# Kernel optimization log

Measured on AMD Instinct MI355X. Metric: run time of the kernel, lower is better.

## Reference

```python
import jax, jax.numpy as jnp
import numpy as np

B, T, HID = 1, 256, 2048
H, D = 16, 128
KD = H * D
CONV = 4
MAX_CG = 30
LAMB_LB = 0.25
NORM_EPS = 1e-5


def setup_inputs() -> dict:
    key = jax.random.key(0)
    ks = jax.random.split(key, 10)
    s = 0.02
    init_lamb = float(np.log(np.exp(1.0 - LAMB_LB) - 1.0))  # softplus^-1(1 - lower_bound)
    return {
        "hidden_states": jax.random.normal(ks[0], (B, T, HID), jnp.float32),
        "Wq": jax.random.normal(ks[1], (HID, KD), jnp.float32) * s,
        "Wk": jax.random.normal(ks[2], (HID, KD), jnp.float32) * s,
        "Wv": jax.random.normal(ks[3], (HID, KD), jnp.float32) * s,
        "Wa": jax.random.normal(ks[4], (HID, H), jnp.float32) * s,
        "ba": jnp.full((H,), 2.0, jnp.float32),
        "Wb": jax.random.normal(ks[5], (HID, H), jnp.float32) * s,
        "bb": jnp.zeros((H,), jnp.float32),
        "conv_wq": jax.random.normal(ks[6], (KD, CONV), jnp.float32) * s,
        "conv_wk": jax.random.normal(ks[7], (KD, CONV), jnp.float32) * s,
        "lambda_params": jnp.full((KD,), init_lamb, jnp.float32),
        "o_norm_w": jnp.ones((D,), jnp.float32),
        "Wo": jax.random.normal(ks[8], (KD, HID), jnp.float32) * s,
    }


def short_conv_silu(x, w):
    # depthwise causal conv over time; x [b,t,c], w [c,k]
    k = w.shape[1]
    xp = jnp.pad(x, ((0, 0), (k - 1, 0), (0, 0)))
    t = x.shape[1]
    y = xp[:, 0:t, :] * w[:, 0]
    for i in range(1, k):
        y = y + xp[:, i:i + t, :] * w[:, i]
    return jax.nn.silu(y)


def l2norm(x):
    return x * jax.lax.rsqrt(jnp.sum(x * x, -1, keepdims=True) + 1e-6)


def rmsnorm(x, w):
    return x * jax.lax.rsqrt(jnp.mean(x * x, -1, keepdims=True) + NORM_EPS) * w


def cg_solve(A, b):
    # solve A x = b per (batch, head) with fixed CG iterations, x0 = 0
    matvec = lambda p: jnp.einsum('bhij,bhj->bhi', A, p)
    x0 = jnp.zeros_like(b)
    rs0 = jnp.sum(b * b, -1)

    def body(i, st):
        xc, r, p, rs = st
        Ap = matvec(p)
        alpha = rs / (jnp.sum(p * Ap, -1) + 1e-12)
        xc = xc + alpha[..., None] * p
        r = r - alpha[..., None] * Ap
        rs_n = jnp.sum(r * r, -1)
        p = r + (rs_n / (rs + 1e-12))[..., None] * p
        return xc, r, p, rs_n

    xf, _, _, _ = jax.lax.fori_loop(0, MAX_CG, body, (x0, b, b, rs0))
    return xf


def mesa_recurrence(q, k, v, g, beta, lamb_diag):
    # q,k,v [b,t,h,d]; g,beta [b,t,h]; lamb_diag [h,d,d]
    def step(carry, inp):
        h_kk, h_kv = carry
        qt, kt, vt, gt, bt = inp
        decay = jnp.exp(gt)[..., None, None]
        b_ = bt[..., None, None]
        h_kk = h_kk * decay + b_ * (kt[..., :, None] * kt[..., None, :])
        h_kv = h_kv * decay + b_ * (kt[..., :, None] * vt[..., None, :])
        A = h_kk + lamb_diag[None]
        q_star = cg_solve(A, qt)
        ot = jnp.einsum('bhk,bhkv->bhv', q_star, h_kv)
        return (h_kk, h_kv), ot

    init = (jnp.zeros((B, H, D, D), q.dtype), jnp.zeros((B, H, D, D), q.dtype))
    xs = (q.transpose(1, 0, 2, 3), k.transpose(1, 0, 2, 3), v.transpose(1, 0, 2, 3),
          g.transpose(1, 0, 2), beta.transpose(1, 0, 2))
    _, o = jax.lax.scan(step, init, xs)
    return o.transpose(1, 0, 2, 3)  # [b,t,h,d]


def reference(hidden_states, Wq, Wk, Wv, Wa, ba, Wb, bb, conv_wq, conv_wk,
              lambda_params, o_norm_w, Wo):
    x = hidden_states
    q = short_conv_silu(x @ Wq, conv_wq)
    k = short_conv_silu(x @ Wk, conv_wk)
    v = x @ Wv
    q = l2norm(q.reshape(B, T, H, D))
    k = l2norm(k.reshape(B, T, H, D))
    v = v.reshape(B, T, H, D)
    beta = jax.nn.sigmoid(x @ Wb + bb)          # [b,t,h]
    g = jax.nn.log_sigmoid(x @ Wa + ba)          # [b,t,h]
    lamb = (jax.nn.softplus(lambda_params) + LAMB_LB).reshape(H, D)
    lamb_diag = lamb[:, :, None] * jnp.eye(D, dtype=lamb.dtype)  # [h,d,d]
    o = mesa_recurrence(q, k, v, g, beta, lamb_diag)
    o = rmsnorm(o, o_norm_w)
    o = o.reshape(B, T, KD) @ Wo
    return o
```

## Files before the change

### kernel.cpp

```cpp
#include <hip/hip_runtime.h>
#include <math.h>

#define TT 256
#define HIDDEN 2048
#define NH 16
#define HD 128
#define KDIM 2048
#define NCG 30

typedef _Float16 h4 __attribute__((ext_vector_type(4)));
typedef _Float16 half8 __attribute__((ext_vector_type(8)));
typedef float floatx4 __attribute__((ext_vector_type(4)));

__device__ __forceinline__ half8 cvt8(const float4 x, const float4 y) {
    half8 f;
    f[0] = (_Float16)x.x; f[1] = (_Float16)x.y; f[2] = (_Float16)x.z; f[3] = (_Float16)x.w;
    f[4] = (_Float16)y.x; f[5] = (_Float16)y.y; f[6] = (_Float16)y.z; f[7] = (_Float16)y.w;
    return f;
}

__device__ __forceinline__ void glds16(const void* g, void* l) {
    __builtin_amdgcn_global_load_lds(
        (const __attribute__((address_space(1))) void*)g,
        (__attribute__((address_space(3))) void*)l, 16, 0, 0);
}

#define SBAR() __builtin_amdgcn_sched_barrier(0)

#define ASTR 72
#define GEMM_LDS (3 * 64 * 128 * 4 + 2 * 64 * ASTR * 2)

__global__ __launch_bounds__(256) void gemm_kernel(
    const float* __restrict__ A,
    const float* __restrict__ Wq, const float* __restrict__ Wk,
    const float* __restrict__ Wv,
    const float* __restrict__ Wa, const float* __restrict__ Wb,
    float* __restrict__ C0, float* __restrict__ C1, float* __restrict__ C2,
    const float* __restrict__ ba, const float* __restrict__ bb,
    float* __restrict__ g, float* __restrict__ beta)
{
    extern __shared__ char smem[];
    float* Bf = (float*)smem;
    _Float16* Ash = (_Float16*)(smem + 3 * 64 * 128 * 4);

    const int tid = threadIdx.x, lane = tid & 63, w = tid >> 6;
    const int q = lane >> 4, l16 = lane & 15;

    const int b = blockIdx.x;
    const int xcd = b & 7, gslot = b >> 3;
    int nt, mt;
    if (gslot < 24) { nt = xcd * 6 + (gslot >> 2); mt = gslot & 3; }
    else           { nt = 48;                      mt = xcd; }
    const int mat = nt >> 4;
    const int ntile = nt & 15;
    const int n0 = ntile * 128;
    const float* __restrict__ W = (mat == 0) ? Wq : (mat == 1) ? Wk : (mat == 2) ? Wv : Wa;
    float* __restrict__ C = (mat == 0) ? C0 : (mat == 1) ? C1 : C2;
    const int m0 = mt * 64;

    const int ar = tid >> 2, ac = (tid & 3) * 16;
    const float* __restrict__ Ap = &A[(size_t)(m0 + ar) * KDIM + ac];

    floatx4 acc[4][2] = {};
    float4 a0, a1, a2, a3;
    float bab[16];

    auto stageB = [&](int s, int buf) {
#pragma unroll
        for (int i = 0; i < 8; i++) {
            const int r0 = w * 16 + i * 2;
            const int row = r0 + (lane >> 5);
            const int qr = (r0 >> 3) & 3;
            const int c = (((lane & 31) * 4) + 128 - 8 * qr) & 127;
            glds16(&W[(size_t)(s * 64 + row) * KDIM + n0 + c],
                   &Bf[(buf * 64 + r0) * 128]);
        }
    };
    auto loadA = [&](int s) {
        a0 = *(const float4*)&Ap[s * 64];      a1 = *(const float4*)&Ap[s * 64 + 4];
        a2 = *(const float4*)&Ap[s * 64 + 8];  a3 = *(const float4*)&Ap[s * 64 + 12];
    };
    auto writeA = [&](int buf) {
        *(half8*)&Ash[buf * 64 * ASTR + ar * ASTR + ac] = cvt8(a0, a1);
        *(half8*)&Ash[buf * 64 * ASTR + ar * ASTR + ac + 8] = cvt8(a2, a3);
    };
    auto loadBab = [&](int s) {
        if (w >= 2) return;
        const float* __restrict__ Wsrc = (w == 0) ? Wa : Wb;
        const int hh = lane & 15, ko = lane >> 4;
#pragma unroll
        for (int hf = 0; hf < 2; hf++)
#pragma unroll
            for (int j = 0; j < 8; j++)
                bab[hf * 8 + j] = Wsrc[(size_t)(s * 64 + hf * 32 + ko * 8 + j) * NH + hh];
    };
    auto writeBab = [&](int buf) {
        if (w >= 2) return;
        const int hh = lane & 15, ko = lane >> 4;
        const int col = w * 16 + hh;
        const int cp = (col + 8 * ko) & 127;
#pragma unroll
        for (int hf = 0; hf < 2; hf++)
#pragma unroll
            for (int j = 0; j < 8; j++)
                Bf[(buf * 64 + hf * 32 + ko * 8 + j) * 128 + cp] = bab[hf * 8 + j];
    };

    const int NSTEP = KDIM / 64;

#define GEMM_COMPUTE(BBASE, ABASE)                                                          \
    {                                                                                       \
    const int c0s = (w * 32 + l16 + 8 * q) & 127;                                           \
    const int c1s = (w * 32 + 16 + l16 + 8 * q) & 127;                                      \
    _Pragma("unroll")                                                                       \
    for (int kk = 0; kk < 2; kk++) {                                                        \
        float f0[8], f1[8];                                                                 \
        _Pragma("unroll")                                                                   \
        for (int j = 0; j < 8; j++) {                                                       \
            const int rowb = ((BBASE) + kk * 32 + q * 8 + j) * 128;                         \
            f0[j] = Bf[rowb + c0s];                                                         \
            f1[j] = Bf[rowb + c1s];                                                         \
        }                                                                                   \
        const half8 bf0 = cvt8(*(const float4*)&f0[0], *(const float4*)&f0[4]);             \
        const half8 bf1 = cvt8(*(const float4*)&f1[0], *(const float4*)&f1[4]);             \
        _Pragma("unroll")                                                                   \
        for (int rr = 0; rr < 4; rr++) {                                                    \
            const half8 af = *(const half8*)&Ash[(ABASE) + (rr * 16 + l16) * ASTR + kk * 32 + q * 8]; \
            acc[rr][0] = __builtin_amdgcn_mfma_f32_16x16x32_f16(af, bf0, acc[rr][0], 0, 0, 0); \
            acc[rr][1] = __builtin_amdgcn_mfma_f32_16x16x32_f16(af, bf1, acc[rr][1], 0, 0, 0); \
        }                                                                                   \
    }                                                                                       \
    }

    if (mat == 3) {
        for (int i = tid; i < 2 * 64 * 96; i += 256) {
            const int buf = i / 6144;
            const int rest = i - buf * 6144;
            const int row = rest / 96, c = 32 + (rest - row * 96);
            const int cp = (c + 8 * ((row >> 3) & 3)) & 127;
            Bf[(buf * 64 + row) * 128 + cp] = 0.f;
        }
        loadBab(0); writeBab(0); loadBab(1);
        loadA(0); writeA(0); loadA(1);
        __syncthreads();
        for (int s = 0; s < NSTEP; s++) {
            const int cur = s & 1;
            GEMM_COMPUTE(cur * 64, cur * 64 * ASTR);
            if (s + 1 < NSTEP) {
                writeBab(cur ^ 1);
                if (s + 2 < NSTEP) loadBab(s + 2);
                writeA(cur ^ 1);
                if (s + 2 < NSTEP) loadA(s + 2);
            }
            __syncthreads();
        }
        if (w == 0) {
            const float bav = ba[l16], bbv = bb[l16];
#pragma unroll
            for (int rr = 0; rr < 4; rr++)
#pragma unroll
                for (int r = 0; r < 4; r++) {
                    const int tr = m0 + rr * 16 + q * 4 + r;
                    float z0 = acc[rr][0][r] + bav;
                    g[tr * NH + l16] = fminf(z0, 0.f) - log1pf(__expf(-fabsf(z0)));
                    float z1 = acc[rr][1][r] + bbv;
                    beta[tr * NH + l16] = 1.f / (1.f + __expf(-z1));
                }
        }
        return;
    }

    stageB(0, 0);
    SBAR();
    loadA(0); writeA(0);
    SBAR();
    loadA(1);
    SBAR();
    stageB(1, 1);
    SBAR();

    for (int s = 0; s < NSTEP; s++) {
        if (s < NSTEP - 1) { asm volatile("s_waitcnt vmcnt(12) lgkmcnt(0)" ::: "memory"); }
        else               { asm volatile("s_waitcnt vmcnt(0) lgkmcnt(0)" ::: "memory"); }
        SBAR();
        __builtin_amdgcn_s_barrier();
        SBAR();
        if (s + 1 < NSTEP) writeA((s + 1) & 1);
        SBAR();
        if (s + 2 < NSTEP) loadA(s + 2);
        SBAR();
        if (s + 2 < NSTEP) stageB(s + 2, (s + 2) % 3);
        GEMM_COMPUTE((s % 3) * 64, (s & 1) * 64 * ASTR);
    }

#pragma unroll
    for (int rr = 0; rr < 4; rr++)
#pragma unroll
        for (int r = 0; r < 4; r++) {
            const int row = m0 + rr * 16 + q * 4 + r;
            C[(size_t)row * KDIM + n0 + w * 32 + l16] = acc[rr][0][r];
            C[(size_t)row * KDIM + n0 + w * 32 + 16 + l16] = acc[rr][1][r];
        }
#undef GEMM_COMPUTE
}

__global__ __launch_bounds__(256) void gemm64_kernel(
    const float* __restrict__ A, const float* __restrict__ Wo,
    float* __restrict__ C)
{
    __shared__ __align__(16) float Bf[3][64][64];
    __shared__ __align__(16) _Float16 Ash[2][32 * ASTR];

    const int tid = threadIdx.x, lane = tid & 63, w = tid >> 6;
    const int q = lane >> 4, l16 = lane & 15;
    const int b = blockIdx.x;
    const int xcd = b & 7, gslot = b >> 3;
    const int nt = xcd * 4 + (gslot >> 3), mt = gslot & 7;
    const int n0 = nt * 64, m0 = mt * 32;

    const int ar = tid >> 3, ac = (tid & 7) * 8;
    const float* __restrict__ Ap = &A[(size_t)(m0 + ar) * KDIM + ac];

    floatx4 acc0 = {}, acc1 = {};
    float4 ax, ay;

    auto stageB = [&](int s, int buf) {
#pragma unroll
        for (int i = 0; i < 4; i++) {
            const int r0 = w * 16 + i * 4;
            const int row = r0 + (lane >> 4);
            const int qr = (r0 >> 3) & 3;
            const int c = (((lane & 15) * 4) + 64 - 8 * qr) & 63;
            glds16(&Wo[(size_t)(s * 64 + row) * KDIM + n0 + c],
                   &Bf[buf][r0][0]);
        }
    };
    auto loadA = [&](int s) {
        ax = *(const float4*)&Ap[s * 64];
        ay = *(const float4*)&Ap[s * 64 + 4];
    };
    auto writeA = [&](int buf) {
        *(half8*)&Ash[buf][ar * ASTR + ac] = cvt8(ax, ay);
    };

    stageB(0, 0);
    SBAR();
    loadA(0); writeA(0);
    SBAR();
    loadA(1);
    SBAR();
    stageB(1, 1);
    SBAR();

    const int NSTEP = KDIM / 64;
    for (int s = 0; s < NSTEP; s++) {
        if (s < NSTEP - 1) { asm volatile("s_waitcnt vmcnt(6) lgkmcnt(0)" ::: "memory"); }
        else               { asm volatile("s_waitcnt vmcnt(0) lgkmcnt(0)" ::: "memory"); }
        SBAR();
        __builtin_amdgcn_s_barrier();
        SBAR();
        if (s + 1 < NSTEP) writeA((s + 1) & 1);
        SBAR();
        if (s + 2 < NSTEP) loadA(s + 2);
        SBAR();
        if (s + 2 < NSTEP) stageB(s + 2, (s + 2) % 3);
        const int bb = s % 3, ab = s & 1;
        const int c0s = (w * 16 + l16 + 8 * q) & 63;
#pragma unroll
        for (int kk = 0; kk < 2; kk++) {
            float f[8];
#pragma unroll
            for (int j = 0; j < 8; j++)
                f[j] = Bf[bb][kk * 32 + q * 8 + j][c0s];
            const half8 bf  = cvt8(*(const float4*)&f[0], *(const float4*)&f[4]);
            const half8 af0 = *(const half8*)&Ash[ab][l16 * ASTR + kk * 32 + q * 8];
            const half8 af1 = *(const half8*)&Ash[ab][(16 + l16) * ASTR + kk * 32 + q * 8];
            acc0 = __builtin_amdgcn_mfma_f32_16x16x32_f16(af0, bf, acc0, 0, 0, 0);
            acc1 = __builtin_amdgcn_mfma_f32_16x16x32_f16(af1, bf, acc1, 0, 0, 0);
        }
    }

#pragma unroll
    for (int r = 0; r < 4; r++) {
        C[(size_t)(m0 + q * 4 + r) * KDIM + n0 + w * 16 + l16] = acc0[r];
        C[(size_t)(m0 + 16 + q * 4 + r) * KDIM + n0 + w * 16 + l16] = acc1[r];
    }
}

__global__ __launch_bounds__(256) void conv_silu_l2_kernel(
    const float* __restrict__ q_pre, const float* __restrict__ k_pre,
    const float* __restrict__ cwq, const float* __restrict__ cwk,
    float* __restrict__ qn, float* __restrict__ kn)
{
    const int t = blockIdx.x, h = blockIdx.y;
    const int which = threadIdx.x >> 7, d = threadIdx.x & 127;
    const int w = threadIdx.x >> 6;
    const int c = h * HD + d;
    const float* pre = which ? k_pre : q_pre;
    const float* cw  = which ? cwk : cwq;
    float y = 0.f;
#pragma unroll
    for (int i = 0; i < 4; i++) {
        const int ts = t - 3 + i;
        if (ts >= 0) y = fmaf(pre[ts * KDIM + c], cw[c * 4 + i], y);
    }
    const float s = y / (1.f + __expf(-y));
    float v = s * s;
#pragma unroll
    for (int off = 32; off > 0; off >>= 1) v += __shfl_down(v, off, 64);
    __shared__ float red[4];
    if ((threadIdx.x & 63) == 0) red[w] = v;
    __syncthreads();
    const float sum = red[which * 2] + red[which * 2 + 1];
    float* dst = which ? kn : qn;
    dst[t * KDIM + c] = s * rsqrtf(sum + 1e-6f);
}

#define PSTR 136
#define YSTR 264

template<int SMAX>
__device__ __forceinline__ void mesa_cg(
    const float* __restrict__ qn, const float* __restrict__ kn, const float* __restrict__ vv,
    const float* __restrict__ g, const float* __restrict__ bet, const float* __restrict__ lp,
    const float* __restrict__ onw, float* __restrict__ out,
    int h, int t0, _Float16* Psh, _Float16* Ysh, float* red,
    float* Gsh, float* bets)
{
    constexpr int NSUB1 = SMAX / 64;
    constexpr int NK2   = SMAX / 32;

    const int tid = threadIdx.x, lane = tid & 63, w = tid >> 6;
    const int quad = lane >> 4, l16 = lane & 15;
    const int tmy = t0 + l16;
    const int dbase = w * 32;

    {
        float sc = g[tid * NH + h];
#pragma unroll
        for (int off = 1; off < 64; off <<= 1) {
            const float o = __shfl_up(sc, off, 64);
            if (lane >= off) sc += o;
        }
        if (lane == 63) red[w] = sc;
        bets[tid] = bet[tid * NH + h];
        __syncthreads();
        float woff = 0.f;
        for (int u = 0; u < w; u++) woff += red[u];
        Gsh[tid] = sc + woff;
        __syncthreads();
    }

    half8 K1[NSUB1][4];
#pragma unroll
    for (int ii = 0; ii < NSUB1; ii++) {
        const int srow = 16 * (w + 4 * ii) + l16;
        const float* kp = &kn[(srow * NH + h) * HD];
#pragma unroll
        for (int kk = 0; kk < 4; kk++) {
            const float4 a = *(const float4*)&kp[kk * 32 + quad * 8];
            const float4 b = *(const float4*)&kp[kk * 32 + quad * 8 + 4];
            K1[ii][kk] = cvt8(a, b);
        }
    }

    half8 KtF[2][NK2];
#pragma unroll
    for (int ss = 0; ss < 2; ss++) {
        const int d = dbase + ss * 16 + l16;
#pragma unroll
        for (int kk = 0; kk < NK2; kk++) {
#pragma unroll
            for (int j = 0; j < 8; j++) {
                const int s = kk * 32 + quad * 8 + j;
                KtF[ss][kk][j] = (_Float16)kn[(s * NH + h) * HD + d];
            }
        }
    }

    half8 Vf[NK2][2];
#pragma unroll
    for (int kk = 0; kk < NK2; kk++) {
#pragma unroll
        for (int ss = 0; ss < 2; ss++) {
            const int dv = dbase + ss * 16 + l16;
#pragma unroll
            for (int j = 0; j < 8; j++) {
                const int s = kk * 32 + quad * 8 + j;
                Vf[kk][ss][j] = (_Float16)vv[(s * NH + h) * HD + dv];
            }
        }
    }

    const float Gt = Gsh[tmy];
    float Wm[NSUB1][4];
#pragma unroll
    for (int ii = 0; ii < NSUB1; ii++)
#pragma unroll
        for (int r = 0; r < 4; r++) {
            const int s = 16 * (w + 4 * ii) + quad * 4 + r;
            Wm[ii][r] = (s <= tmy) ? bets[s] * __expf(Gt - Gsh[s]) : 0.f;
        }
    float lam[8], xv[8], rv[8], pv[8];
#pragma unroll
    for (int ss = 0; ss < 2; ss++)
#pragma unroll
        for (int r = 0; r < 4; r++) {
            const int e = ss * 4 + r;
            const int d = dbase + ss * 16 + quad * 4 + r;
            const float lx = lp[h * HD + d];
            lam[e] = fmaxf(lx, 0.f) + log1pf(__expf(-fabsf(lx))) + 0.25f;
            const float b = qn[(tmy * NH + h) * HD + d];
            xv[e] = 0.f; rv[e] = b; pv[e] = b;
        }
    float rs = 0.f;
#pragma unroll
    for (int e = 0; e < 8; e++) rs += rv[e] * rv[e];
    rs += __shfl_xor(rs, 16, 64); rs += __shfl_xor(rs, 32, 64);

    auto writeP = [&](const float* src) {
#pragma unroll
        for (int ss = 0; ss < 2; ss++) {
            h4 ph;
            ph.x = (_Float16)src[ss * 4 + 0]; ph.y = (_Float16)src[ss * 4 + 1];
            ph.z = (_Float16)src[ss * 4 + 2]; ph.w = (_Float16)src[ss * 4 + 3];
            *(h4*)&Psh[l16 * PSTR + dbase + ss * 16 + quad * 4] = ph;
        }
    };
    writeP(pv);

    for (int it = 0; it <= NCG; it++) {
        __syncthreads();
        floatx4 acc1a[NSUB1] = {}, acc1b[NSUB1] = {};
#pragma unroll
        for (int kk = 0; kk < 2; kk++) {
            const half8 bfa = *(const half8*)&Psh[l16 * PSTR + kk * 32 + quad * 8];
            const half8 bfb = *(const half8*)&Psh[l16 * PSTR + (kk + 2) * 32 + quad * 8];
#pragma unroll
            for (int ii = 0; ii < NSUB1; ii++) {
                acc1a[ii] = __builtin_amdgcn_mfma_f32_16x16x32_f16(K1[ii][kk], bfa, acc1a[ii], 0, 0, 0);
                acc1b[ii] = __builtin_amdgcn_mfma_f32_16x16x32_f16(K1[ii][kk + 2], bfb, acc1b[ii], 0, 0, 0);
            }
        }
#pragma unroll
        for (int ii = 0; ii < NSUB1; ii++) {
            h4 yh;
            yh.x = (_Float16)(Wm[ii][0] * (acc1a[ii][0] + acc1b[ii][0]));
            yh.y = (_Float16)(Wm[ii][1] * (acc1a[ii][1] + acc1b[ii][1]));
            yh.z = (_Float16)(Wm[ii][2] * (acc1a[ii][2] + acc1b[ii][2]));
            yh.w = (_Float16)(Wm[ii][3] * (acc1a[ii][3] + acc1b[ii][3]));
            *(h4*)&Ysh[l16 * YSTR + 16 * (w + 4 * ii) + quad * 4] = yh;
        }
        __syncthreads();
        if (it == NCG) break;

        floatx4 acc2a[2] = {}, acc2b[2] = {};
#pragma unroll
        for (int kk = 0; kk < NK2; kk += 2) {
            const half8 bf0 = *(const half8*)&Ysh[l16 * YSTR + kk * 32 + quad * 8];
            const half8 bf1 = *(const half8*)&Ysh[l16 * YSTR + (kk + 1) * 32 + quad * 8];
#pragma unroll
            for (int ss = 0; ss < 2; ss++) {
                acc2a[ss] = __builtin_amdgcn_mfma_f32_16x16x32_f16(KtF[ss][kk], bf0, acc2a[ss], 0, 0, 0);
                acc2b[ss] = __builtin_amdgcn_mfma_f32_16x16x32_f16(KtF[ss][kk + 1], bf1, acc2b[ss], 0, 0, 0);
            }
        }
        float Ap[8], pAp = 0.f;
#pragma unroll
        for (int ss = 0; ss < 2; ss++)
#pragma unroll
            for (int r = 0; r < 4; r++) {
                const int e = ss * 4 + r;
                Ap[e] = (acc2a[ss][r] + acc2b[ss][r]) + lam[e] * pv[e];
                pAp = fmaf(pv[e], Ap[e], pAp);
            }
        pAp += __shfl_xor(pAp, 16, 64); pAp += __shfl_xor(pAp, 32, 64);
        const float alpha = rs / (pAp + 1e-12f);
        float rsn = 0.f;
#pragma unroll
        for (int e = 0; e < 8; e++) {
            xv[e] = fmaf(alpha, pv[e], xv[e]);
            rv[e] = fmaf(-alpha, Ap[e], rv[e]);
            rsn = fmaf(rv[e], rv[e], rsn);
        }
        rsn += __shfl_xor(rsn, 16, 64); rsn += __shfl_xor(rsn, 32, 64);
        const float bcg = rsn / (rs + 1e-12f);
#pragma unroll
        for (int e = 0; e < 8; e++) pv[e] = fmaf(bcg, pv[e], rv[e]);
        rs = rsn;
        writeP(it == NCG - 1 ? xv : pv);
    }

    floatx4 accOa[2] = {}, accOb[2] = {};
#pragma unroll
    for (int kk = 0; kk < NK2; kk += 2) {
        const half8 af0 = *(const half8*)&Ysh[l16 * YSTR + kk * 32 + quad * 8];
        const half8 af1 = *(const half8*)&Ysh[l16 * YSTR + (kk + 1) * 32 + quad * 8];
#pragma unroll
        for (int ss = 0; ss < 2; ss++) {
            accOa[ss] = __builtin_amdgcn_mfma_f32_16x16x32_f16(af0, Vf[kk][ss], accOa[ss], 0, 0, 0);
            accOb[ss] = __builtin_amdgcn_mfma_f32_16x16x32_f16(af1, Vf[kk + 1][ss], accOb[ss], 0, 0, 0);
        }
    }
    float accO[2][4];
#pragma unroll
    for (int ss = 0; ss < 2; ss++)
#pragma unroll
        for (int r = 0; r < 4; r++) accO[ss][r] = accOa[ss][r] + accOb[ss][r];

    float part[4];
#pragma unroll
    for (int r = 0; r < 4; r++) {
        part[r] = accO[0][r] * accO[0][r] + accO[1][r] * accO[1][r];
#pragma unroll
        for (int off = 1; off < 16; off <<= 1) part[r] += __shfl_xor(part[r], off, 64);
    }
    if (l16 == 0) {
#pragma unroll
        for (int r = 0; r < 4; r++) red[w * 16 + quad * 4 + r] = part[r];
    }
    __syncthreads();
    const float w0 = onw[dbase + l16], w1 = onw[dbase + 16 + l16];
#pragma unroll
    for (int r = 0; r < 4; r++) {
        const int qr = quad * 4 + r;
        const float sumd = red[qr] + red[16 + qr] + red[32 + qr] + red[48 + qr];
        const float sc = rsqrtf(sumd * (1.f / HD) + 1e-5f);
        const int trow = ((t0 + qr) * NH + h) * HD;
        out[trow + dbase + l16] = accO[0][r] * sc * w0;
        out[trow + dbase + 16 + l16] = accO[1][r] * sc * w1;
    }
}

__global__ __launch_bounds__(256, 1) void mesa_kernel(
    const float* __restrict__ qn, const float* __restrict__ kn, const float* __restrict__ vv,
    const float* __restrict__ g, const float* __restrict__ bet, const float* __restrict__ lp,
    const float* __restrict__ onw, float* __restrict__ out)
{
    __shared__ __align__(16) _Float16 Psh[16 * PSTR];
    __shared__ __align__(16) _Float16 Ysh[16 * YSTR];
    __shared__ float red[64];
    __shared__ float Gsh[256];
    __shared__ float bets[256];
    const int h = blockIdx.x, jb = blockIdx.y, t0 = jb * 16;
    switch (jb >> 2) {
        case 0:  mesa_cg<64> (qn, kn, vv, g, bet, lp, onw, out, h, t0, Psh, Ysh, red, Gsh, bets); break;
        case 1:  mesa_cg<128>(qn, kn, vv, g, bet, lp, onw, out, h, t0, Psh, Ysh, red, Gsh, bets); break;
        case 2:  mesa_cg<192>(qn, kn, vv, g, bet, lp, onw, out, h, t0, Psh, Ysh, red, Gsh, bets); break;
        default: mesa_cg<256>(qn, kn, vv, g, bet, lp, onw, out, h, t0, Psh, Ysh, red, Gsh, bets); break;
    }
}

extern "C" void kernel_launch(void* const* d_in, const int* in_sizes, int n_in,
                              void* d_out, int out_size, void* d_ws, size_t ws_size,
                              hipStream_t stream)
{
    (void)in_sizes; (void)n_in; (void)out_size; (void)ws_size;
    const float* x   = (const float*)d_in[0];
    const float* Wq  = (const float*)d_in[1];
    const float* Wk  = (const float*)d_in[2];
    const float* Wv  = (const float*)d_in[3];
    const float* Wa  = (const float*)d_in[4];
    const float* ba  = (const float*)d_in[5];
    const float* Wb  = (const float*)d_in[6];
    const float* bb  = (const float*)d_in[7];
    const float* cwq = (const float*)d_in[8];
    const float* cwk = (const float*)d_in[9];
    const float* lp  = (const float*)d_in[10];
    const float* onw = (const float*)d_in[11];
    const float* Wo  = (const float*)d_in[12];

    char* wsb = (char*)d_ws;
    float* q_pre = (float*)wsb;
    float* k_pre = q_pre + 524288;
    float* v     = k_pre + 524288;
    float* qn    = v + 524288;
    float* kn    = qn + 524288;
    float* g     = kn + 524288;
    float* beta  = g + 4096;
    float* onorm = q_pre;
    float* outp  = (float*)d_out;

    (void)hipFuncSetAttribute((const void*)gemm_kernel,
                              hipFuncAttributeMaxDynamicSharedMemorySize, GEMM_LDS);
    gemm_kernel<<<dim3(196), 256, GEMM_LDS, stream>>>(x, Wq, Wk, Wv, Wa, Wb,
                                                      q_pre, k_pre, v, ba, bb, g, beta);
    conv_silu_l2_kernel<<<dim3(TT, NH), 256, 0, stream>>>(q_pre, k_pre, cwq, cwk, qn, kn);

    mesa_kernel<<<dim3(NH, 16), 256, 0, stream>>>(qn, kn, v, g, beta, lp, onw, onorm);

    gemm64_kernel<<<dim3(256), 256, 0, stream>>>(onorm, Wo, outp);
}
```

Measured before the change: 228.7 us.

## Fuse causal conv, SiLU and L2 norm into the mesa CG kernel

Removes the separate conv_silu_l2 kernel and recomputes the short convolution, SiLU and L2 normalisation of k (for rows up to SMAX) and q (for the block's 16 rows) inside each mesa block. The normalised k is staged as fp16 in dynamic LDS and q as fp32 in LDS, so the normalised tensors are never written to or read back from global memory and one launch disappears. In exchange every block redundantly recomputes k's convolution with a serial two-pass loop per row, which adds latency at the start of each block, and LDS use grows considerably.

After: 267.5 us. 1.17x slower.

```diff
diff --git a/kernel.cpp b/kernel.cpp
--- a/kernel.cpp
+++ b/kernel.cpp
@@ -287,45 +287,24 @@
     }
 }
 
-__global__ __launch_bounds__(256) void conv_silu_l2_kernel(
-    const float* __restrict__ q_pre, const float* __restrict__ k_pre,
-    const float* __restrict__ cwq, const float* __restrict__ cwk,
-    float* __restrict__ qn, float* __restrict__ kn)
-{
-    const int t = blockIdx.x, h = blockIdx.y;
-    const int which = threadIdx.x >> 7, d = threadIdx.x & 127;
-    const int w = threadIdx.x >> 6;
-    const int c = h * HD + d;
-    const float* pre = which ? k_pre : q_pre;
-    const float* cw  = which ? cwk : cwq;
-    float y = 0.f;
-#pragma unroll
-    for (int i = 0; i < 4; i++) {
-        const int ts = t - 3 + i;
-        if (ts >= 0) y = fmaf(pre[ts * KDIM + c], cw[c * 4 + i], y);
-    }
-    const float s = y / (1.f + __expf(-y));
-    float v = s * s;
-#pragma unroll
-    for (int off = 32; off > 0; off >>= 1) v += __shfl_down(v, off, 64);
-    __shared__ float red[4];
-    if ((threadIdx.x & 63) == 0) red[w] = v;
-    __syncthreads();
-    const float sum = red[which * 2] + red[which * 2 + 1];
-    float* dst = which ? kn : qn;
-    dst[t * KDIM + c] = s * rsqrtf(sum + 1e-6f);
-}
-
 #define PSTR 136
 #define YSTR 264
+#define KNBS 136
+#define QNBS 132
+#define MESA_LDS (256 * KNBS * 2 + 16 * QNBS * 4 + 16 * PSTR * 2 + 16 * YSTR * 2 \
+                  + 64 * 4 + 256 * 4 + 256 * 4 + 16 * 17 * 4)
 
 template<int SMAX>
 __device__ __forceinline__ void mesa_cg(
-    const float* __restrict__ qn, const float* __restrict__ kn, const float* __restrict__ vv,
-    const float* __restrict__ g, const float* __restrict__ bet, const float* __restrict__ lp,
-    const float* __restrict__ onw, float* __restrict__ out,
-    int h, int t0, _Float16* Psh, _Float16* Ysh, float* red,
-    float* Gsh, float* bets)
+    const float* __restrict__ q_pre, const float* __restrict__ k_pre,
+    const float* __restrict__ vv,
+    const float* __restrict__ cwq, const float* __restrict__ cwk,
+    const float* __restrict__ g, const float* __restrict__ bet,
+    const float* __restrict__ lp, const float* __restrict__ onw,
+    float* __restrict__ out,
+    int h, int t0,
+    _Float16* KNB, float* QNB, _Float16* Psh, _Float16* Ysh,
+    float* red, float* Gsh, float* bets, float* qred)
 {
     constexpr int NSUB1 = SMAX / 64;
     constexpr int NK2   = SMAX / 32;
@@ -351,17 +330,90 @@
         __syncthreads();
     }
 
+    {
+        const float* kbase = &k_pre[h * HD];
+        const float* cwkh = &cwk[h * HD * 4];
+        if (tid < SMAX) {
+            const int r = tid;
+            float ssum = 0.f;
+#pragma unroll 1
+            for (int pass = 0; pass < 2; pass++) {
+                const float scl = (pass == 0) ? 0.f : rsqrtf(ssum + 1e-6f);
+#pragma unroll 1
+                for (int d0 = 0; d0 < HD; d0 += 4) {
+                    float wc0[4], wc1[4], wc2[4], wc3[4];
+                    *(float4*)wc0 = *(const float4*)&cwkh[(d0 + 0) * 4];
+                    *(float4*)wc1 = *(const float4*)&cwkh[(d0 + 1) * 4];
+                    *(float4*)wc2 = *(const float4*)&cwkh[(d0 + 2) * 4];
+                    *(float4*)wc3 = *(const float4*)&cwkh[(d0 + 3) * 4];
+                    float y0 = 0.f, y1 = 0.f, y2 = 0.f, y3 = 0.f;
+#pragma unroll
+                    for (int i = 0; i < 4; i++) {
+                        const int ts = r - 3 + i;
+                        if (ts >= 0) {
+                            const float4 xv = *(const float4*)&kbase[(size_t)ts * KDIM + d0];
+                            y0 = fmaf(xv.x, wc0[i], y0);
+                            y1 = fmaf(xv.y, wc1[i], y1);
+                            y2 = fmaf(xv.z, wc2[i], y2);
+                            y3 = fmaf(xv.w, wc3[i], y3);
+                        }
+                    }
+                    y0 = y0 / (1.f + __expf(-y0));
+                    y1 = y1 / (1.f + __expf(-y1));
+                    y2 = y2 / (1.f + __expf(-y2));
+                    y3 = y3 / (1.f + __expf(-y3));
+                    if (pass == 0) {
+                        ssum = fmaf(y0, y0, fmaf(y1, y1, fmaf(y2, y2, fmaf(y3, y3, ssum))));
+                    } else {
+                        h4 o;
+                        o.x = (_Float16)(y0 * scl); o.y = (_Float16)(y1 * scl);
+                        o.z = (_Float16)(y2 * scl); o.w = (_Float16)(y3 * scl);
+                        *(h4*)&KNB[r * KNBS + d0] = o;
+                    }
+                }
+            }
+        }
+    }
+    float qy[8];
+    {
+        const float* qbase = &q_pre[h * HD];
+        const float* cwqh = &cwq[h * HD * 4];
+        const int qr_ = tid >> 4, qd = (tid & 15) * 8;
+        const int tq = t0 + qr_;
+        float psum = 0.f;
+#pragma unroll
+        for (int j = 0; j < 8; j++) {
+            float acc = 0.f;
+#pragma unroll
+            for (int i = 0; i < 4; i++) {
+                const int ts = tq - 3 + i;
+                if (ts >= 0)
+                    acc = fmaf(qbase[(size_t)ts * KDIM + qd + j], cwqh[(qd + j) * 4 + i], acc);
+            }
+            qy[j] = acc / (1.f + __expf(-acc));
+            psum = fmaf(qy[j], qy[j], psum);
+        }
+        qred[qr_ * 17 + (tid & 15)] = psum;
+    }
+    __syncthreads();
+    {
+        const int qr_ = tid >> 4, qd = (tid & 15) * 8;
+        float rsum = 0.f;
+#pragma unroll
+        for (int u = 0; u < 16; u++) rsum += qred[qr_ * 17 + u];
+        const float scq = rsqrtf(rsum + 1e-6f);
+#pragma unroll
+        for (int j = 0; j < 8; j++) QNB[qr_ * QNBS + qd + j] = qy[j] * scq;
+    }
+    __syncthreads();
+
     half8 K1[NSUB1][4];
 #pragma unroll
     for (int ii = 0; ii < NSUB1; ii++) {
         const int srow = 16 * (w + 4 * ii) + l16;
-        const float* kp = &kn[(srow * NH + h) * HD];
-#pragma unroll
-        for (int kk = 0; kk < 4; kk++) {
-            const float4 a = *(const float4*)&kp[kk * 32 + quad * 8];
-            const float4 b = *(const float4*)&kp[kk * 32 + quad * 8 + 4];
-            K1[ii][kk] = cvt8(a, b);
-        }
+#pragma unroll
+        for (int kk = 0; kk < 4; kk++)
+            K1[ii][kk] = *(const half8*)&KNB[srow * KNBS + kk * 32 + quad * 8];
     }
 
     half8 KtF[2][NK2];
@@ -373,7 +425,7 @@
 #pragma unroll
             for (int j = 0; j < 8; j++) {
                 const int s = kk * 32 + quad * 8 + j;
-                KtF[ss][kk][j] = (_Float16)kn[(s * NH + h) * HD + d];
+                KtF[ss][kk][j] = KNB[s * KNBS + d];
             }
         }
     }
@@ -410,7 +462,7 @@
             const int d = dbase + ss * 16 + quad * 4 + r;
             const float lx = lp[h * HD + d];
             lam[e] = fmaxf(lx, 0.f) + log1pf(__expf(-fabsf(lx))) + 0.25f;
-            const float b = qn[(tmy * NH + h) * HD + d];
+            const float b = QNB[l16 * QNBS + d];
             xv[e] = 0.f; rv[e] = b; pv[e] = b;
         }
     float rs = 0.f;
@@ -533,21 +585,29 @@
 }
 
 __global__ __launch_bounds__(256, 1) void mesa_kernel(
-    const float* __restrict__ qn, const float* __restrict__ kn, const float* __restrict__ vv,
-    const float* __restrict__ g, const float* __restrict__ bet, const float* __restrict__ lp,
-    const float* __restrict__ onw, float* __restrict__ out)
+    const float* __restrict__ q_pre, const float* __restrict__ k_pre,
+    const float* __restrict__ vv,
+    const float* __restrict__ cwq, const float* __restrict__ cwk,
+    const float* __restrict__ g, const float* __restrict__ bet,
+    const float* __restrict__ lp, const float* __restrict__ onw,
+    float* __restrict__ out)
 {
-    __shared__ __align__(16) _Float16 Psh[16 * PSTR];
-    __shared__ __align__(16) _Float16 Ysh[16 * YSTR];
-    __shared__ float red[64];
-    __shared__ float Gsh[256];
-    __shared__ float bets[256];
+    extern __shared__ char smem_raw[];
+    char* p = smem_raw;
+    _Float16* KNB = (_Float16*)p;             p += 256 * KNBS * 2;
+    float* QNB    = (float*)p;                p += 16 * QNBS * 4;
+    _Float16* Psh = (_Float16*)p;             p += 16 * PSTR * 2;
+    _Float16* Ysh = (_Float16*)p;             p += 16 * YSTR * 2;
+    float* red    = (float*)p;                p += 64 * 4;
+    float* Gsh    = (float*)p;                p += 256 * 4;
+    float* bets   = (float*)p;                p += 256 * 4;
+    float* qred   = (float*)p;
     const int h = blockIdx.x, jb = blockIdx.y, t0 = jb * 16;
     switch (jb >> 2) {
-        case 0:  mesa_cg<64> (qn, kn, vv, g, bet, lp, onw, out, h, t0, Psh, Ysh, red, Gsh, bets); break;
-        case 1:  mesa_cg<128>(qn, kn, vv, g, bet, lp, onw, out, h, t0, Psh, Ysh, red, Gsh, bets); break;
-        case 2:  mesa_cg<192>(qn, kn, vv, g, bet, lp, onw, out, h, t0, Psh, Ysh, red, Gsh, bets); break;
-        default: mesa_cg<256>(qn, kn, vv, g, bet, lp, onw, out, h, t0, Psh, Ysh, red, Gsh, bets); break;
+        case 0:  mesa_cg<64> (q_pre, k_pre, vv, cwq, cwk, g, bet, lp, onw, out, h, t0, KNB, QNB, Psh, Ysh, red, Gsh, bets, qred); break;
+        case 1:  mesa_cg<128>(q_pre, k_pre, vv, cwq, cwk, g, bet, lp, onw, out, h, t0, KNB, QNB, Psh, Ysh, red, Gsh, bets, qred); break;
+        case 2:  mesa_cg<192>(q_pre, k_pre, vv, cwq, cwk, g, bet, lp, onw, out, h, t0, KNB, QNB, Psh, Ysh, red, Gsh, bets, qred); break;
+        default: mesa_cg<256>(q_pre, k_pre, vv, cwq, cwk, g, bet, lp, onw, out, h, t0, KNB, QNB, Psh, Ysh, red, Gsh, bets, qred); break;
     }
 }
 
@@ -574,20 +634,21 @@
     float* q_pre = (float*)wsb;
     float* k_pre = q_pre + 524288;
     float* v     = k_pre + 524288;
-    float* qn    = v + 524288;
-    float* kn    = qn + 524288;
-    float* g     = kn + 524288;
+    float* onorm = v + 524288;
+    float* g     = onorm + 524288;
     float* beta  = g + 4096;
-    float* onorm = q_pre;
     float* outp  = (float*)d_out;
 
     (void)hipFuncSetAttribute((const void*)gemm_kernel,
                               hipFuncAttributeMaxDynamicSharedMemorySize, GEMM_LDS);
+    (void)hipFuncSetAttribute((const void*)mesa_kernel,
+                              hipFuncAttributeMaxDynamicSharedMemorySize, MESA_LDS);
+
     gemm_kernel<<<dim3(196), 256, GEMM_LDS, stream>>>(x, Wq, Wk, Wv, Wa, Wb,
                                                       q_pre, k_pre, v, ba, bb, g, beta);
-    conv_silu_l2_kernel<<<dim3(TT, NH), 256, 0, stream>>>(q_pre, k_pre, cwq, cwk, qn, kn);
-
-    mesa_kernel<<<dim3(NH, 16), 256, 0, stream>>>(qn, kn, v, g, beta, lp, onw, onorm);
+
+    mesa_kernel<<<dim3(NH, 16), 256, MESA_LDS, stream>>>(q_pre, k_pre, v, cwq, cwk,
+                                                         g, beta, lp, onw, onorm);
 
     gemm64_kernel<<<dim3(256), 256, 0, stream>>>(onorm, Wo, outp);
 }
```
